# Optimization experiments

Measured on AMD Instinct MI355X. Metric: run time of the kernel, lower is better.

The kernel has to match this reference:

```python
import jax, jax.numpy as jnp
import numpy as np

DIM = 768
HEADS = 12
HEAD_DIM = DIM // HEADS
HIDDEN = int(DIM * 4.0)


def setup_inputs() -> dict:
    key = jax.random.key(0)
    ks = jax.random.split(key, 12)
    s = lambda *shape: 0.02
    inp = {
        "x": jax.random.normal(ks[0], (8, 1024, DIM), dtype=jnp.float32),
        "norm1_g": jnp.ones((DIM,), jnp.float32),
        "norm1_b": jnp.zeros((DIM,), jnp.float32),
        "qkv_w": jax.random.normal(ks[1], (DIM, 3 * DIM), jnp.float32) * 0.02,
        "qkv_b": jnp.zeros((3 * DIM,), jnp.float32),
        "proj_w": jax.random.normal(ks[2], (DIM, DIM), jnp.float32) * 0.02,
        "proj_b": jnp.zeros((DIM,), jnp.float32),
        "norm2_g": jnp.ones((DIM,), jnp.float32),
        "norm2_b": jnp.zeros((DIM,), jnp.float32),
        "fc1_w": jax.random.normal(ks[3], (DIM, HIDDEN), jnp.float32) * 0.02,
        "fc1_b": jnp.zeros((HIDDEN,), jnp.float32),
        "fc2_w": jax.random.normal(ks[4], (HIDDEN, DIM), jnp.float32) * 0.02,
        "fc2_b": jnp.zeros((DIM,), jnp.float32),
    }
    return inp


def _layernorm(x, g, b, eps=1e-5):
    mu = jnp.mean(x, axis=-1, keepdims=True)
    var = jnp.mean(jnp.square(x - mu), axis=-1, keepdims=True)
    return (x - mu) * jax.lax.rsqrt(var + eps) * g + b


def _attention(x, qkv_w, qkv_b, proj_w, proj_b):
    B, N, C = x.shape
    qkv = x @ qkv_w + qkv_b                      # [B, N, 3C]
    qkv = qkv.reshape(B, N, 3, HEADS, HEAD_DIM)
    q, k, v = jnp.moveaxis(qkv, 2, 0)            # each [B, N, H, D]
    scale = HEAD_DIM ** -0.5
    scores = jnp.einsum("bnhd,bmhd->bhnm", q, k) * scale  # [B, H, N, N]
    attn = jax.nn.softmax(scores, axis=-1)
    out = jnp.einsum("bhnm,bmhd->bnhd", attn, v).reshape(B, N, C)
    return out @ proj_w + proj_b


def reference(x, norm1_g, norm1_b, qkv_w, qkv_b, proj_w, proj_b,
              norm2_g, norm2_b, fc1_w, fc1_b, fc2_w, fc2_b):
    # Pre-norm transformer block (inference: DropPath = identity)
    x = x + _attention(_layernorm(x, norm1_g, norm1_b), qkv_w, qkv_b, proj_w, proj_b)
    h = _layernorm(x, norm2_g, norm2_b)
    h = jax.nn.gelu(h @ fc1_w + fc1_b, approximate=False) @ fc2_w + fc2_b
    return x + h
```

## Files before the change

kernel.cpp:

```cpp
#include <hip/hip_runtime.h>

typedef __attribute__((ext_vector_type(8))) short s16x8;
typedef __attribute__((ext_vector_type(4))) short s16x4;
typedef __attribute__((ext_vector_type(4))) float f32x4;

static __device__ __forceinline__ short f2bf(float f) {
    unsigned u = __builtin_bit_cast(unsigned, f);
    u = (u + 0x7FFFu + ((u >> 16) & 1u)) >> 16;
    return (short)u;
}

__device__ __forceinline__ void gload16(const short* g, short* l) {
    __builtin_amdgcn_global_load_lds(
        (const __attribute__((address_space(1))) void*)g,
        (__attribute__((address_space(3))) void*)l,
        16, 0, 0);
}

__global__ __launch_bounds__(256) void transpose_convert(
    const float* __restrict__ W, short* __restrict__ Wt, int K, int N)
{
    __shared__ float tile[32][33];
    const int bx = blockIdx.x * 32;
    const int by = blockIdx.y * 32;
    const int tx = threadIdx.x;
    const int ty = threadIdx.y;
    for (int i = 0; i < 32; i += 8)
        tile[ty + i][tx] = W[(size_t)(by + ty + i) * N + bx + tx];
    __syncthreads();
    for (int i = 0; i < 32; i += 8)
        Wt[(size_t)(bx + ty + i) * K + by + tx] = f2bf(tile[tx][ty + i]);
}

__global__ __launch_bounds__(256) void layernorm_kernel(
    const float* __restrict__ x, const float* __restrict__ g,
    const float* __restrict__ b, short* __restrict__ out)
{
    const int row = blockIdx.x;
    const float* xr = x + (size_t)row * 768;
    const int t = threadIdx.x;
    float v0 = xr[t], v1 = xr[t + 256], v2 = xr[t + 512];
    __shared__ float red[4];

    float s = v0 + v1 + v2;
    for (int off = 32; off >= 1; off >>= 1) s += __shfl_down(s, off, 64);
    if ((t & 63) == 0) red[t >> 6] = s;
    __syncthreads();
    const float mean = (red[0] + red[1] + red[2] + red[3]) * (1.0f / 768.0f);
    const float d0 = v0 - mean, d1 = v1 - mean, d2 = v2 - mean;
    __syncthreads();
    float ss = d0 * d0 + d1 * d1 + d2 * d2;
    for (int off = 32; off >= 1; off >>= 1) ss += __shfl_down(ss, off, 64);
    if ((t & 63) == 0) red[t >> 6] = ss;
    __syncthreads();
    const float var = (red[0] + red[1] + red[2] + red[3]) * (1.0f / 768.0f);
    const float rstd = rsqrtf(var + 1e-5f);
    out[(size_t)row * 768 + t]       = f2bf(d0 * rstd * g[t] + b[t]);
    out[(size_t)row * 768 + t + 256] = f2bf(d1 * rstd * g[t + 256] + b[t + 256]);
    out[(size_t)row * 768 + t + 512] = f2bf(d2 * rstd * g[t + 512] + b[t + 512]);
}

#define G_STAGE(AS, BS)                                                     \
    {                                                                       \
        _Pragma("unroll") for (int c = 0; c < 4; c++) {                     \
            gload16(aP[c], &AS[(w * 4 + c) * 512]); aP[c] += 64;            \
        }                                                                   \
        _Pragma("unroll") for (int c = 0; c < 2; c++) {                     \
            gload16(bP[c], &BS[(w * 2 + c) * 512]); bP[c] += 64;            \
        }                                                                   \
    }

#define G_COMPUTE(AS, BS)                                                   \
    {                                                                       \
        s16x8 af[4][2], bf[2][2];                                           \
        _Pragma("unroll") for (int m = 0; m < 4; m++) {                     \
            const int rbase = (wr + m * 16 + fr) * 64;                      \
            af[m][0] = *(const s16x8*)&AS[rbase + ((g ^ sl) * 8)];          \
            af[m][1] = *(const s16x8*)&AS[rbase + (((4 + g) ^ sl) * 8)];    \
        }                                                                   \
        _Pragma("unroll") for (int n = 0; n < 2; n++) {                     \
            const int rbase = (wc + n * 16 + fr) * 64;                      \
            bf[n][0] = *(const s16x8*)&BS[rbase + ((g ^ sl) * 8)];          \
            bf[n][1] = *(const s16x8*)&BS[rbase + (((4 + g) ^ sl) * 8)];    \
        }                                                                   \
        _Pragma("unroll") for (int m = 0; m < 4; m++)                       \
            _Pragma("unroll") for (int n = 0; n < 2; n++) {                 \
                acc[m][n] = __builtin_amdgcn_mfma_f32_16x16x32_bf16(af[m][0], bf[n][0], acc[m][n], 0, 0, 0); \
                acc[m][n] = __builtin_amdgcn_mfma_f32_16x16x32_bf16(af[m][1], bf[n][1], acc[m][n], 0, 0, 0); \
            }                                                               \
    }

template <int MODE>
__global__ __launch_bounds__(256) void gemm_bt_db(
    const short* __restrict__ A, const short* __restrict__ Bt,
    const float* __restrict__ bias, const float* __restrict__ res,
    void* __restrict__ out, short* __restrict__ vtout, int M, int N, int K)
{
    __shared__ __align__(16) short As0[128 * 64];
    __shared__ __align__(16) short As1[128 * 64];
    __shared__ __align__(16) short Bs0[64 * 64];
    __shared__ __align__(16) short Bs1[64 * 64];

    const int t = threadIdx.x;
    const int l = t & 63;
    const int w = t >> 6;
    const int wr = (w >> 1) * 64;
    const int wc = (w & 1) * 32;

    const int ncol = N >> 6;
    const int xcd = blockIdx.x & 7;
    const int idx = blockIdx.x >> 3;
    const int tn = (idx % ncol) << 6;
    const int tm = ((idx / ncol) * 8 + xcd) << 7;

    const int srow = l >> 3;
    const int scol = ((l & 7) ^ srow) * 8;
    const short* aP[4]; const short* bP[2];
#pragma unroll
    for (int c = 0; c < 4; c++)
        aP[c] = A  + (size_t)(tm + (w * 4 + c) * 8 + srow) * K + scol;
#pragma unroll
    for (int c = 0; c < 2; c++)
        bP[c] = Bt + (size_t)(tn + (w * 2 + c) * 8 + srow) * K + scol;

    const int fr = l & 15;
    const int g = l >> 4;
    const int sl = fr & 7;

    f32x4 acc[4][2] = {};

    G_STAGE(As0, Bs0);
    __syncthreads();

    const int half = K >> 7;
    for (int it = 0; it < half; ++it) {
        G_STAGE(As1, Bs1);
        G_COMPUTE(As0, Bs0);
        __syncthreads();
        if (it < half - 1) G_STAGE(As0, Bs0);
        G_COMPUTE(As1, Bs1);
        __syncthreads();
    }

    const int fq = g * 4;
#pragma unroll
    for (int m = 0; m < 4; m++) {
#pragma unroll
        for (int n = 0; n < 2; n++) {
            const int col = tn + wc + n * 16 + fr;
            const float bv = bias[col];
            if (MODE == 3 && col >= 1536) {
                const int row0 = tm + wr + m * 16 + fq;
                const int bb = row0 >> 10;
                const int nseq = row0 & 1023;
                s16x4 ov;
#pragma unroll
                for (int j = 0; j < 4; j++) ov[j] = f2bf(acc[m][n][j] + bv);
                *(s16x4*)(vtout + (((size_t)(bb * 768 + (col - 1536))) << 10) + nseq) = ov;
            } else {
#pragma unroll
                for (int j = 0; j < 4; j++) {
                    const int row = tm + wr + m * 16 + fq + j;
                    float v = acc[m][n][j] + bv;
                    if (MODE == 2) {
                        const float u = v * (0.7978845608f + 0.0356774081f * v * v);
                        const float e = __builtin_amdgcn_exp2f(u * 2.8853900817779268f);
                        v = v - v * __builtin_amdgcn_rcpf(e + 1.0f);
                    }
                    if (MODE == 1) {
                        ((float*)out)[(size_t)row * N + col] = v + res[(size_t)row * N + col];
                    } else {
                        ((short*)out)[(size_t)row * N + col] = f2bf(v);
                    }
                }
            }
        }
    }
}

#define ATTN_STAGE(KS, VS)                                                  \
    {                                                                       \
        gload16(kP,                    &KS[w * 1024]);                      \
        gload16(kP + (size_t)8 * 2304, &KS[w * 1024 + 512]);                \
        gload16(vP,                    &VS[w * 1024]);                      \
        gload16(vP + (size_t)8 * 1024, &VS[w * 1024 + 512]);                \
        kP += (size_t)64 * 2304;                                            \
        vP += 64;                                                           \
    }

#define ATTN_COMPUTE(KS, VS)                                                \
    {                                                                       \
        s16x8 ka[4][2];                                                     \
        _Pragma("unroll") for (int n = 0; n < 4; n++) {                     \
            const int rbase = (n * 16 + lq) * 64;                           \
            ka[n][0] = *(const s16x8*)&KS[rbase + ((g * 8) ^ swz)];         \
            ka[n][1] = *(const s16x8*)&KS[rbase + ((32 + g * 8) ^ swz)];    \
        }                                                                   \
        f32x4 s[2][4];                                                      \
        _Pragma("unroll") for (int r = 0; r < 2; r++)                       \
            _Pragma("unroll") for (int n = 0; n < 4; n++) {                 \
                f32x4 sv = {};                                              \
                sv = __builtin_amdgcn_mfma_f32_16x16x32_bf16(ka[n][0], qb[r][0], sv, 0, 0, 0); \
                sv = __builtin_amdgcn_mfma_f32_16x16x32_bf16(ka[n][1], qb[r][1], sv, 0, 0, 0); \
                s[r][n] = sv;                                               \
            }                                                               \
        s16x8 va[4][2];                                                     \
        _Pragma("unroll") for (int dt = 0; dt < 4; dt++) {                  \
            const int rbase = (dt * 16 + lq) * 64;                          \
            va[dt][0] = *(const s16x8*)&VS[rbase + ((g * 8) ^ swz)];        \
            va[dt][1] = *(const s16x8*)&VS[rbase + ((32 + g * 8) ^ swz)];   \
        }                                                                   \
        _Pragma("unroll") for (int r = 0; r < 2; r++) {                     \
            float mx = fmaxf(fmaxf(s[r][0][0], s[r][0][1]), fmaxf(s[r][0][2], s[r][0][3])); \
            _Pragma("unroll") for (int n = 1; n < 4; n++)                   \
                mx = fmaxf(mx, fmaxf(fmaxf(s[r][n][0], s[r][n][1]), fmaxf(s[r][n][2], s[r][n][3]))); \
            const float mxs = mx * kSc;                                     \
            if (!__all(mxs - m_run[r] <= 8.0f)) {                           \
                float gm = mxs;                                             \
                gm = fmaxf(gm, __shfl_xor(gm, 16, 64));                     \
                gm = fmaxf(gm, __shfl_xor(gm, 32, 64));                     \
                const float mnew = fmaxf(m_run[r], gm);                     \
                const float alpha = __builtin_amdgcn_exp2f(m_run[r] - mnew);\
                m_run[r] = mnew;                                            \
                l_run[r] *= alpha;                                          \
                _Pragma("unroll") for (int dt = 0; dt < 4; dt++) {          \
                    acc[r][dt][0] *= alpha; acc[r][dt][1] *= alpha;         \
                    acc[r][dt][2] *= alpha; acc[r][dt][3] *= alpha;         \
                }                                                           \
            }                                                               \
            const float mb = m_run[r];                                      \
            float ssum = 0.f;                                               \
            _Pragma("unroll") for (int n = 0; n < 4; n++) {                 \
                const float p0 = __builtin_amdgcn_exp2f(s[r][n][0] * kSc - mb); \
                const float p1 = __builtin_amdgcn_exp2f(s[r][n][1] * kSc - mb); \
                const float p2 = __builtin_amdgcn_exp2f(s[r][n][2] * kSc - mb); \
                const float p3 = __builtin_amdgcn_exp2f(s[r][n][3] * kSc - mb); \
                ssum += (p0 + p1) + (p2 + p3);                              \
                unsigned lo, hi;                                            \
                asm("v_cvt_pk_bf16_f32 %0, %1, %2" : "=v"(lo) : "v"(p0), "v"(p1)); \
                asm("v_cvt_pk_bf16_f32 %0, %1, %2" : "=v"(hi) : "v"(p2), "v"(p3)); \
                unsigned* pp = (unsigned*)&Ps[w][r * 16 + lq][n * 16 + g * 4]; \
                pp[0] = lo; pp[1] = hi;                                     \
            }                                                               \
            l_run[r] += ssum;                                               \
        }                                                                   \
        _Pragma("unroll") for (int r = 0; r < 2; r++) {                     \
            const s16x8 pb0 = *(const s16x8*)&Ps[w][r * 16 + lq][g * 8];    \
            const s16x8 pb1 = *(const s16x8*)&Ps[w][r * 16 + lq][32 + g * 8]; \
            _Pragma("unroll") for (int dt = 0; dt < 4; dt++) {              \
                acc[r][dt] = __builtin_amdgcn_mfma_f32_16x16x32_bf16(va[dt][0], pb0, acc[r][dt], 0, 0, 0); \
                acc[r][dt] = __builtin_amdgcn_mfma_f32_16x16x32_bf16(va[dt][1], pb1, acc[r][dt], 0, 0, 0); \
            }                                                               \
        }                                                                   \
    }

__global__ __launch_bounds__(256) void attn_kernel(
    const short* __restrict__ qkv, const short* __restrict__ vTg,
    short* __restrict__ out)
{
    const int bid = blockIdx.x;
    const int x = bid & 7;
    const int i = bid >> 3;
    const int bh = x + 8 * (i % 12);
    const int qt = i / 12;
    const int b = bh / 12, h = bh % 12;

    __shared__ __align__(16) short Ks0[64 * 64];
    __shared__ __align__(16) short Ks1[64 * 64];
    __shared__ __align__(16) short Vs0[64 * 64];
    __shared__ __align__(16) short Vs1[64 * 64];
    __shared__ __align__(16) short Ps[4][32][72];

    const int t = threadIdx.x;
    const int l = t & 63;
    const int w = t >> 6;
    const int lq = l & 15;
    const int g = l >> 4;
    const float kSc = 0.18033688011112042f;

    const int q0 = b * 1024 + qt * 128 + w * 32;

    s16x8 qb[2][2];
#pragma unroll
    for (int r = 0; r < 2; r++) {
        const short* qp = qkv + ((size_t)(q0 + r * 16 + lq)) * 2304 + h * 64 + g * 8;
        qb[r][0] = *(const s16x8*)qp;
        qb[r][1] = *(const s16x8*)(qp + 32);
    }

    const int srow = l >> 3;
    const int scol = ((l & 7) ^ srow) * 8;
    const short* kP = qkv + (size_t)(b * 1024 + w * 16 + srow) * 2304 + 768 + h * 64 + scol;
    const short* vP = vTg + (size_t)(bh * 64 + w * 16 + srow) * 1024 + scol;

    f32x4 acc[2][4] = {};
    float m_run[2] = {-1e30f, -1e30f};
    float l_run[2] = {0.f, 0.f};

    const int swz = (lq & 7) * 8;

    ATTN_STAGE(Ks0, Vs0);
    __syncthreads();

    for (int it = 0; it < 8; ++it) {
        ATTN_STAGE(Ks1, Vs1);
        ATTN_COMPUTE(Ks0, Vs0);
        __syncthreads();
        if (it < 7) ATTN_STAGE(Ks0, Vs0);
        ATTN_COMPUTE(Ks1, Vs1);
        __syncthreads();
    }

#pragma unroll
    for (int r = 0; r < 2; r++) {
        float ls = l_run[r];
        ls += __shfl_xor(ls, 16, 64);
        ls += __shfl_xor(ls, 32, 64);
        const float rinv = 1.0f / ls;
        const int qrow = q0 + r * 16 + lq;
#pragma unroll
        for (int dt = 0; dt < 4; dt++) {
            s16x4 ov;
#pragma unroll
            for (int j = 0; j < 4; j++) ov[j] = f2bf(acc[r][dt][j] * rinv);
            *(s16x4*)(out + (size_t)qrow * 768 + h * 64 + dt * 16 + g * 4) = ov;
        }
    }
}

extern "C" void kernel_launch(void* const* d_in, const int* in_sizes, int n_in,
                              void* d_out, int out_size, void* d_ws, size_t ws_size,
                              hipStream_t stream) {
    const float* x      = (const float*)d_in[0];
    const float* n1g    = (const float*)d_in[1];
    const float* n1b    = (const float*)d_in[2];
    const float* qkv_w  = (const float*)d_in[3];
    const float* qkv_b  = (const float*)d_in[4];
    const float* proj_w = (const float*)d_in[5];
    const float* proj_b = (const float*)d_in[6];
    const float* n2g    = (const float*)d_in[7];
    const float* n2b    = (const float*)d_in[8];
    const float* fc1_w  = (const float*)d_in[9];
    const float* fc1_b  = (const float*)d_in[10];
    const float* fc2_w  = (const float*)d_in[11];
    const float* fc2_b  = (const float*)d_in[12];
    float* out = (float*)d_out;

    char* ws = (char*)d_ws;
    short* qkv_wT  = (short*)(ws + 0);
    short* proj_wT = (short*)(ws + 3538944);
    short* fc1_wT  = (short*)(ws + 4718592);
    short* fc2_wT  = (short*)(ws + 9437184);
    short* bufA    = (short*)(ws + 14155776);
    short* bufB    = (short*)(ws + 26738688);
    short* vT      = (short*)(ws + 64487424);
    float* bufC    = (float*)(ws + 77070336);

    const dim3 tb(32, 8);
    transpose_convert<<<dim3(2304 / 32, 768 / 32), tb, 0, stream>>>(qkv_w, qkv_wT, 768, 2304);
    transpose_convert<<<dim3(768 / 32, 768 / 32),  tb, 0, stream>>>(proj_w, proj_wT, 768, 768);
    transpose_convert<<<dim3(3072 / 32, 768 / 32), tb, 0, stream>>>(fc1_w, fc1_wT, 768, 3072);
    transpose_convert<<<dim3(768 / 32, 3072 / 32), tb, 0, stream>>>(fc2_w, fc2_wT, 3072, 768);

    layernorm_kernel<<<8192, 256, 0, stream>>>(x, n1g, n1b, bufA);

    gemm_bt_db<3><<<64 * (2304 / 64), 256, 0, stream>>>(
        bufA, qkv_wT, qkv_b, nullptr, bufB, vT, 8192, 2304, 768);

    attn_kernel<<<768, 256, 0, stream>>>(bufB, vT, bufA);

    gemm_bt_db<1><<<64 * (768 / 64), 256, 0, stream>>>(
        bufA, proj_wT, proj_b, x, bufC, nullptr, 8192, 768, 768);

    layernorm_kernel<<<8192, 256, 0, stream>>>(bufC, n2g, n2b, bufA);

    gemm_bt_db<2><<<64 * (3072 / 64), 256, 0, stream>>>(
        bufA, fc1_wT, fc1_b, nullptr, bufB, nullptr, 8192, 3072, 768);

    gemm_bt_db<1><<<64 * (768 / 64), 256, 0, stream>>>(
        bufB, fc2_wT, fc2_b, bufC, out, nullptr, 8192, 768, 3072);
}
```

Before: 254.2 us.

## Add 256x256-tile 8-wave pipelined GEMM for QKV and FC1 projections

Adds a new GEMM kernel with 256x256 output tiles, 512 threads and double-buffered LDS. Its K loop is split into four phases that interleave staged global-to-LDS loads, barriers with explicit waitcnt, and MFMA bursts run at raised priority. The kernel replaces the 128x64-tile GEMM for the QKV and FC1 launches, aiming for more operand reuse per LDS load and better overlap of memory with compute. The old kernel is reduced to the residual-add path used by proj and FC2. The larger tile uses much more LDS and registers per block, and the K loop is hardcoded for K=768, so fewer blocks run at once.

```diff
diff --git a/kernel.cpp b/kernel.cpp
--- a/kernel.cpp
+++ b/kernel.cpp
@@ -60,6 +60,165 @@
     out[(size_t)row * 768 + t + 512] = f2bf(d2 * rstd * g[t + 512] + b[t + 512]);
 }
 
+#define PSYNC_(n)                                                           \
+    asm volatile("s_waitcnt vmcnt(" #n ")" ::: "memory");                   \
+    __builtin_amdgcn_s_barrier();                                           \
+    asm volatile("s_waitcnt lgkmcnt(0)" ::: "memory");                      \
+    __builtin_amdgcn_sched_barrier(0);
+#define PSYNC(n) PSYNC_(n)
+
+#define STG2(P, DST)                                                        \
+    { gload16(P[0], (DST) + stg); gload16(P[1], (DST) + stg + 512);         \
+      P[0] += 64; P[1] += 64; }
+
+#define DSA(CA, MB)                                                         \
+    _Pragma("unroll") for (int mf = 0; mf < 4; mf++) {                      \
+        af[mf][0] = *(const s16x8*)&CA[arow + (MB + mf) * 1024 + cc0];      \
+        af[mf][1] = *(const s16x8*)&CA[arow + (MB + mf) * 1024 + cc1];      \
+    }
+
+#define DSB(CB, BREG, NB)                                                   \
+    _Pragma("unroll") for (int nf = 0; nf < 2; nf++) {                      \
+        BREG[nf][0] = *(const s16x8*)&CB[brow + (NB + nf) * 1024 + cc0];    \
+        BREG[nf][1] = *(const s16x8*)&CB[brow + (NB + nf) * 1024 + cc1];    \
+    }
+
+#define MM8(BREG, MB, NB)                                                   \
+    _Pragma("unroll") for (int mf = 0; mf < 4; mf++)                        \
+    _Pragma("unroll") for (int nf = 0; nf < 2; nf++) {                      \
+        acc[MB + mf][NB + nf] = __builtin_amdgcn_mfma_f32_16x16x32_bf16(    \
+            af[mf][0], BREG[nf][0], acc[MB + mf][NB + nf], 0, 0, 0);        \
+        acc[MB + mf][NB + nf] = __builtin_amdgcn_mfma_f32_16x16x32_bf16(    \
+            af[mf][1], BREG[nf][1], acc[MB + mf][NB + nf], 0, 0, 0);        \
+    }
+
+#define TILE8(CA, CB, S0, S1, S2, S3, VM3)                                  \
+    do {                                                                    \
+        DSA(CA, 0); DSB(CB, b01, 0);                                        \
+        S0;                                                                 \
+        PSYNC(6);                                                           \
+        __builtin_amdgcn_s_setprio(1); MM8(b01, 0, 0);                      \
+        __builtin_amdgcn_s_setprio(0);                                      \
+        __builtin_amdgcn_s_barrier();                                       \
+        DSB(CB, b23, 2);                                                    \
+        S1;                                                                 \
+        PSYNC(6);                                                           \
+        __builtin_amdgcn_s_setprio(1); MM8(b23, 0, 2);                      \
+        __builtin_amdgcn_s_setprio(0);                                      \
+        __builtin_amdgcn_s_barrier();                                       \
+        DSA(CA, 4);                                                         \
+        S2;                                                                 \
+        PSYNC(6);                                                           \
+        __builtin_amdgcn_s_setprio(1); MM8(b23, 4, 2);                      \
+        __builtin_amdgcn_s_setprio(0);                                      \
+        __builtin_amdgcn_s_barrier();                                       \
+        S3;                                                                 \
+        PSYNC(VM3);                                                         \
+        __builtin_amdgcn_s_setprio(1); MM8(b01, 4, 0);                      \
+        __builtin_amdgcn_s_setprio(0);                                      \
+        __builtin_amdgcn_s_barrier();                                       \
+    } while (0)
+
+template <int MODE>
+__global__ __launch_bounds__(512, 2) void gemm_8ph(
+    const short* __restrict__ A, const short* __restrict__ Bt,
+    const float* __restrict__ bias, void* __restrict__ out,
+    short* __restrict__ vtout, int M, int N, int K)
+{
+    __shared__ __align__(16) short As0[256 * 64];
+    __shared__ __align__(16) short As1[256 * 64];
+    __shared__ __align__(16) short Bs0[256 * 64];
+    __shared__ __align__(16) short Bs1[256 * 64];
+
+    const int t = threadIdx.x;
+    const int l = t & 63;
+    const int w = t >> 6;
+    const int wm = w >> 2;
+    const int wn = w & 3;
+
+    const int ncol = N >> 8;
+    const int xcd = blockIdx.x & 7;
+    const int idx = blockIdx.x >> 3;
+    const int tn = (idx % ncol) << 8;
+    const int tm = ((idx / ncol) * 8 + xcd) << 8;
+
+    const int srow = l >> 3;
+    const int scol = ((l & 7) ^ srow) * 8;
+    const short* pAT[2]; const short* pAB[2];
+    const short* pBL[2]; const short* pBR[2];
+#pragma unroll
+    for (int c = 0; c < 2; c++) {
+        pAT[c] = A  + (size_t)(tm +       (2 * w + c) * 8 + srow) * K + scol;
+        pAB[c] = A  + (size_t)(tm + 128 + (2 * w + c) * 8 + srow) * K + scol;
+        pBL[c] = Bt + (size_t)(tn +       (2 * w + c) * 8 + srow) * K + scol;
+        pBR[c] = Bt + (size_t)(tn + 128 + (2 * w + c) * 8 + srow) * K + scol;
+    }
+    const int stg = w * 1024;
+
+    const int fr = l & 15;
+    const int g  = l >> 4;
+    const int sl = fr & 7;
+    const int arow = (wm * 128 + fr) * 64;
+    const int brow = (wn * 64 + fr) * 64;
+    const int cc0 = (g ^ sl) * 8;
+    const int cc1 = ((4 + g) ^ sl) * 8;
+
+    f32x4 acc[8][4] = {};
+    s16x8 af[4][2], b01[2][2], b23[2][2];
+
+    STG2(pBL, Bs0);
+    STG2(pBR, Bs0 + 8192);
+    STG2(pAT, As0);
+    STG2(pAB, As0 + 8192);
+    STG2(pBL, Bs1);
+    STG2(pBR, Bs1 + 8192);
+    asm volatile("s_waitcnt vmcnt(4)" ::: "memory");
+    __builtin_amdgcn_s_barrier();
+
+#pragma unroll 1
+    for (int rep = 0; rep < 5; ++rep) {
+        TILE8(As0, Bs0,
+              STG2(pAT, As1), STG2(pAB, As1 + 8192),
+              STG2(pBL, Bs0), STG2(pBR, Bs0 + 8192), 4);
+        TILE8(As1, Bs1,
+              STG2(pAT, As0), STG2(pAB, As0 + 8192),
+              STG2(pBL, Bs1), STG2(pBR, Bs1 + 8192), 4);
+    }
+    TILE8(As0, Bs0,
+          STG2(pAT, As1), STG2(pAB, As1 + 8192), (void)0, (void)0, 0);
+    TILE8(As1, Bs1, (void)0, (void)0, (void)0, (void)0, 0);
+
+#pragma unroll
+    for (int mf = 0; mf < 8; mf++) {
+#pragma unroll
+        for (int nf = 0; nf < 4; nf++) {
+            const int col = tn + wn * 64 + nf * 16 + fr;
+            const float bv = bias[col];
+            if (MODE == 3 && col >= 1536) {
+                const int row0 = tm + wm * 128 + mf * 16 + g * 4;
+                const int bb = row0 >> 10;
+                const int nseq = row0 & 1023;
+                s16x4 ov;
+#pragma unroll
+                for (int j = 0; j < 4; j++) ov[j] = f2bf(acc[mf][nf][j] + bv);
+                *(s16x4*)(vtout + (((size_t)(bb * 768 + (col - 1536))) << 10) + nseq) = ov;
+            } else {
+#pragma unroll
+                for (int j = 0; j < 4; j++) {
+                    const int row = tm + wm * 128 + mf * 16 + g * 4 + j;
+                    float v = acc[mf][nf][j] + bv;
+                    if (MODE == 2) {
+                        const float u = v * (0.7978845608f + 0.0356774081f * v * v);
+                        const float e = __builtin_amdgcn_exp2f(u * 2.8853900817779268f);
+                        v = v - v * __builtin_amdgcn_rcpf(e + 1.0f);
+                    }
+                    ((short*)out)[(size_t)row * N + col] = f2bf(v);
+                }
+            }
+        }
+    }
+}
+
 #define G_STAGE(AS, BS)                                                     \
     {                                                                       \
         _Pragma("unroll") for (int c = 0; c < 4; c++) {                     \
@@ -72,29 +231,28 @@
 
 #define G_COMPUTE(AS, BS)                                                   \
     {                                                                       \
-        s16x8 af[4][2], bf[2][2];                                           \
+        s16x8 gaf[4][2], gbf[2][2];                                         \
         _Pragma("unroll") for (int m = 0; m < 4; m++) {                     \
             const int rbase = (wr + m * 16 + fr) * 64;                      \
-            af[m][0] = *(const s16x8*)&AS[rbase + ((g ^ sl) * 8)];          \
-            af[m][1] = *(const s16x8*)&AS[rbase + (((4 + g) ^ sl) * 8)];    \
+            gaf[m][0] = *(const s16x8*)&AS[rbase + ((g ^ sl) * 8)];         \
+            gaf[m][1] = *(const s16x8*)&AS[rbase + (((4 + g) ^ sl) * 8)];   \
         }                                                                   \
         _Pragma("unroll") for (int n = 0; n < 2; n++) {                     \
             const int rbase = (wc + n * 16 + fr) * 64;                      \
-            bf[n][0] = *(const s16x8*)&BS[rbase + ((g ^ sl) * 8)];          \
-            bf[n][1] = *(const s16x8*)&BS[rbase + (((4 + g) ^ sl) * 8)];    \
+            gbf[n][0] = *(const s16x8*)&BS[rbase + ((g ^ sl) * 8)];         \
+            gbf[n][1] = *(const s16x8*)&BS[rbase + (((4 + g) ^ sl) * 8)];   \
         }                                                                   \
         _Pragma("unroll") for (int m = 0; m < 4; m++)                       \
             _Pragma("unroll") for (int n = 0; n < 2; n++) {                 \
-                acc[m][n] = __builtin_amdgcn_mfma_f32_16x16x32_bf16(af[m][0], bf[n][0], acc[m][n], 0, 0, 0); \
-                acc[m][n] = __builtin_amdgcn_mfma_f32_16x16x32_bf16(af[m][1], bf[n][1], acc[m][n], 0, 0, 0); \
+                acc[m][n] = __builtin_amdgcn_mfma_f32_16x16x32_bf16(gaf[m][0], gbf[n][0], acc[m][n], 0, 0, 0); \
+                acc[m][n] = __builtin_amdgcn_mfma_f32_16x16x32_bf16(gaf[m][1], gbf[n][1], acc[m][n], 0, 0, 0); \
             }                                                               \
     }
 
-template <int MODE>
 __global__ __launch_bounds__(256) void gemm_bt_db(
     const short* __restrict__ A, const short* __restrict__ Bt,
     const float* __restrict__ bias, const float* __restrict__ res,
-    void* __restrict__ out, short* __restrict__ vtout, int M, int N, int K)
+    float* __restrict__ out, int M, int N, int K)
 {
     __shared__ __align__(16) short As0[128 * 64];
     __shared__ __align__(16) short As1[128 * 64];
@@ -149,30 +307,10 @@
         for (int n = 0; n < 2; n++) {
             const int col = tn + wc + n * 16 + fr;
             const float bv = bias[col];
-            if (MODE == 3 && col >= 1536) {
-                const int row0 = tm + wr + m * 16 + fq;
-                const int bb = row0 >> 10;
-                const int nseq = row0 & 1023;
-                s16x4 ov;
-#pragma unroll
-                for (int j = 0; j < 4; j++) ov[j] = f2bf(acc[m][n][j] + bv);
-                *(s16x4*)(vtout + (((size_t)(bb * 768 + (col - 1536))) << 10) + nseq) = ov;
-            } else {
-#pragma unroll
-                for (int j = 0; j < 4; j++) {
-                    const int row = tm + wr + m * 16 + fq + j;
-                    float v = acc[m][n][j] + bv;
-                    if (MODE == 2) {
-                        const float u = v * (0.7978845608f + 0.0356774081f * v * v);
-                        const float e = __builtin_amdgcn_exp2f(u * 2.8853900817779268f);
-                        v = v - v * __builtin_amdgcn_rcpf(e + 1.0f);
-                    }
-                    if (MODE == 1) {
-                        ((float*)out)[(size_t)row * N + col] = v + res[(size_t)row * N + col];
-                    } else {
-                        ((short*)out)[(size_t)row * N + col] = f2bf(v);
-                    }
-                }
+#pragma unroll
+            for (int j = 0; j < 4; j++) {
+                const int row = tm + wr + m * 16 + fq + j;
+                out[(size_t)row * N + col] = acc[m][n][j] + bv + res[(size_t)row * N + col];
             }
         }
     }
@@ -364,19 +502,19 @@
 
     layernorm_kernel<<<8192, 256, 0, stream>>>(x, n1g, n1b, bufA);
 
-    gemm_bt_db<3><<<64 * (2304 / 64), 256, 0, stream>>>(
-        bufA, qkv_wT, qkv_b, nullptr, bufB, vT, 8192, 2304, 768);
+    gemm_8ph<3><<<(8192 / 256) * (2304 / 256), 512, 0, stream>>>(
+        bufA, qkv_wT, qkv_b, bufB, vT, 8192, 2304, 768);
 
     attn_kernel<<<768, 256, 0, stream>>>(bufB, vT, bufA);
 
-    gemm_bt_db<1><<<64 * (768 / 64), 256, 0, stream>>>(
-        bufA, proj_wT, proj_b, x, bufC, nullptr, 8192, 768, 768);
+    gemm_bt_db<<<64 * (768 / 64), 256, 0, stream>>>(
+        bufA, proj_wT, proj_b, x, bufC, 8192, 768, 768);
 
     layernorm_kernel<<<8192, 256, 0, stream>>>(bufC, n2g, n2b, bufA);
 
-    gemm_bt_db<2><<<64 * (3072 / 64), 256, 0, stream>>>(
-        bufA, fc1_wT, fc1_b, nullptr, bufB, nullptr, 8192, 3072, 768);
-
-    gemm_bt_db<1><<<64 * (768 / 64), 256, 0, stream>>>(
-        bufB, fc2_wT, fc2_b, bufC, out, nullptr, 8192, 768, 3072);
-}
+    gemm_8ph<2><<<(8192 / 256) * (3072 / 256), 512, 0, stream>>>(
+        bufA, fc1_wT, fc1_b, bufB, nullptr, 8192, 3072, 768);
+
+    gemm_bt_db<<<64 * (768 / 64), 256, 0, stream>>>(
+        bufB, fc2_wT, fc2_b, bufC, out, 8192, 768, 3072);
+}
```

Measured after the change: 265.8 us. 1.05x slower.
